# Performance work log

Measured on AMD Instinct MI355X. Metric: run time of the kernel, lower is better.

The kernel has to match this reference:

```python
import jax, jax.numpy as jnp
import numpy as np

N_NODES = 10000
N_EDGES = 160000
D_IN = 512
D_OUT = 512

def setup_inputs() -> dict:
    key = jax.random.key(0)
    k1, k2, k3, k4, k5 = jax.random.split(key, 5)
    feature = jax.random.normal(k1, (N_NODES, D_IN), dtype=jnp.float32)
    src = jax.random.randint(k2, (N_EDGES,), 0, N_NODES, dtype=jnp.int64)
    dst = jax.random.randint(k3, (N_EDGES,), 0, N_NODES, dtype=jnp.int64)
    # Linear(2*in_feats -> out_feats): stored as [2*D_IN, D_OUT] for x @ W + b
    W = jax.random.normal(k4, (2 * D_IN, D_OUT), dtype=jnp.float32) * (1.0 / np.sqrt(2 * D_IN))
    b = jax.random.normal(k5, (D_OUT,), dtype=jnp.float32) * 0.01
    return {"feature": feature, "src": src, "dst": dst, "W": W, "b": b}

def reference(feature, src, dst, W, b):
    n = feature.shape[0]
    # update_all(copy_src('h'), sum -> 'neigh'): scatter-add src features onto dst
    neigh = jax.ops.segment_sum(feature[src], dst, num_segments=n)  # [N, D_IN]
    # in_degrees(): count of incoming edges per node
    degs = jax.ops.segment_sum(jnp.ones_like(dst, dtype=feature.dtype), dst, num_segments=n)
    # clamp to 1 to avoid 0/0 for isolated nodes (sum is 0 there, so result is 0 either way)
    hk_neigh = neigh / jnp.maximum(degs, 1.0)[:, None]
    hk = jnp.concatenate([feature, hk_neigh], axis=-1) @ W + b  # [N, D_OUT]
    return jax.nn.relu(hk)
```

## Files before the change

kernel.cpp:

```cpp
#include <hip/hip_runtime.h>
#include <hip/hip_bf16.h>


#define N_NODES 10000
#define N_EDGES 160000
#define D_IN    512
#define D_OUT   512
#define K_DIM   1024

typedef float  f32x4  __attribute__((ext_vector_type(4)));
typedef __bf16 bf16x8 __attribute__((ext_vector_type(8)));
typedef unsigned short us8 __attribute__((ext_vector_type(8)));
typedef unsigned short us4 __attribute__((ext_vector_type(4)));

__device__ __forceinline__ unsigned short f2b(float f) {
    unsigned int u = __float_as_uint(f);
    unsigned int r = u + 0x7FFFu + ((u >> 16) & 1u);
    return (unsigned short)(r >> 16);
}
__device__ __forceinline__ float b2f(unsigned short h) {
    return __uint_as_float(((unsigned int)h) << 16);
}
__device__ __forceinline__ void gl_lds16(const void* g, void* l) {
    auto gp = (const __attribute__((address_space(1))) unsigned int*)(uintptr_t)g;
    auto lp = (__attribute__((address_space(3))) unsigned int*)(uintptr_t)l;
    __builtin_amdgcn_global_load_lds(gp, lp, 16, 0, 0);
}

__global__ __launch_bounds__(256) void wtrans_kernel(const float* __restrict__ W,
                                                     unsigned short* __restrict__ WbT,
                                                     int* __restrict__ cnt) {
    const int kt = blockIdx.x;
    const int nt = blockIdx.y;
    const int t  = threadIdx.x;

    const int bid = nt * 32 + kt;
    const int zi  = bid * 20 + t;
    if (t < 20 && zi < N_NODES) cnt[zi] = 0;

    __shared__ float tile[32][33];
    const int c  = t & 31;
    const int r0 = t >> 5;
#pragma unroll
    for (int p = 0; p < 4; ++p) {
        int r = r0 + p * 8;
        tile[r][c] = W[(size_t)(kt * 32 + r) * D_OUT + nt * 32 + c];
    }
    __syncthreads();
#pragma unroll
    for (int p = 0; p < 4; ++p) {
        int r = r0 + p * 8;
        WbT[(size_t)(nt * 32 + r) * K_DIM + kt * 32 + c] = f2b(tile[c][r]);
    }
}

__global__ __launch_bounds__(256) void convert_hist_kernel(const float* __restrict__ feat,
                                                           const int* __restrict__ dst,
                                                           unsigned short* __restrict__ Xb,
                                                           int* __restrict__ cnt) {
    const int gid = blockIdx.x * 256 + threadIdx.x;
    const int row = gid >> 6;
    const int l   = gid & 63;
    const float4* s = (const float4*)(feat + (size_t)row * D_IN + l * 8);
    float4 v0 = s[0], v1 = s[1];
    us8 o;
    o[0] = f2b(v0.x); o[1] = f2b(v0.y); o[2] = f2b(v0.z); o[3] = f2b(v0.w);
    o[4] = f2b(v1.x); o[5] = f2b(v1.y); o[6] = f2b(v1.z); o[7] = f2b(v1.w);
    *(us8*)(Xb + (size_t)row * K_DIM + l * 8) = o;
    if (gid < N_EDGES) atomicAdd(&cnt[dst[gid]], 1);
}

__global__ __launch_bounds__(256) void scan_kernel(const int* __restrict__ cnt,
                                                   int* __restrict__ rowstart,
                                                   int* __restrict__ cursor) {
    __shared__ int sums[256];
    const int t = threadIdx.x;
    const int base = t * 40;
    const int4* c4 = (const int4*)(cnt + base);
    int s = 0;
    if (base < N_NODES) {
#pragma unroll
        for (int i = 0; i < 10; ++i) {
            int4 v = c4[i];
            s += v.x + v.y + v.z + v.w;
        }
    }
    sums[t] = s;
    __syncthreads();
    for (int off = 1; off < 256; off <<= 1) {
        int v = (t >= off) ? sums[t - off] : 0;
        __syncthreads();
        sums[t] += v;
        __syncthreads();
    }
    int run = (t == 0) ? 0 : sums[t - 1];
    if (base < N_NODES) {
        int4* r4 = (int4*)(rowstart + base);
        int4* u4 = (int4*)(cursor + base);
#pragma unroll
        for (int i = 0; i < 10; ++i) {
            int4 v = c4[i];
            int4 o;
            o.x = run;  o.y = run + v.x;  o.z = run + v.x + v.y;
            o.w = run + v.x + v.y + v.z;
            run += v.x + v.y + v.z + v.w;
            r4[i] = o;
            u4[i] = o;
        }
    }
    if (t == 255) rowstart[N_NODES] = sums[255];
}

__global__ __launch_bounds__(256) void bucket_kernel(const int* __restrict__ src,
                                                     const int* __restrict__ dst,
                                                     int* __restrict__ cursor,
                                                     int* __restrict__ eidx) {
    int e = blockIdx.x * 256 + threadIdx.x;
    int d = dst[e];
    int slot = atomicAdd(&cursor[d], 1);
    eidx[slot] = src[e];
}

__global__ __launch_bounds__(256) void gather_kernel(unsigned short* Xb,
                                                     const int* __restrict__ eidx,
                                                     const int* __restrict__ rowstart) {
    const int wv   = threadIdx.x >> 6;
    const int l    = threadIdx.x & 63;
    const int half = (blockIdx.x >= 2500) ? 1 : 0;
    const int b    = blockIdx.x - half * 2500;
    const int node = b * 4 + wv;
    const int col  = half * 256 + l * 4;
    const int beg  = rowstart[node];
    const int end  = rowstart[node + 1];
    float a0 = 0.f, a1 = 0.f, a2 = 0.f, a3 = 0.f;
    int j = beg;
    for (; j + 8 <= end; j += 8) {
        us4 v0 = *(const us4*)(Xb + (size_t)eidx[j]     * K_DIM + col);
        us4 v1 = *(const us4*)(Xb + (size_t)eidx[j + 1] * K_DIM + col);
        us4 v2 = *(const us4*)(Xb + (size_t)eidx[j + 2] * K_DIM + col);
        us4 v3 = *(const us4*)(Xb + (size_t)eidx[j + 3] * K_DIM + col);
        us4 v4 = *(const us4*)(Xb + (size_t)eidx[j + 4] * K_DIM + col);
        us4 v5 = *(const us4*)(Xb + (size_t)eidx[j + 5] * K_DIM + col);
        us4 v6 = *(const us4*)(Xb + (size_t)eidx[j + 6] * K_DIM + col);
        us4 v7 = *(const us4*)(Xb + (size_t)eidx[j + 7] * K_DIM + col);
        a0 += ((b2f(v0[0]) + b2f(v1[0])) + (b2f(v2[0]) + b2f(v3[0])))
            + ((b2f(v4[0]) + b2f(v5[0])) + (b2f(v6[0]) + b2f(v7[0])));
        a1 += ((b2f(v0[1]) + b2f(v1[1])) + (b2f(v2[1]) + b2f(v3[1])))
            + ((b2f(v4[1]) + b2f(v5[1])) + (b2f(v6[1]) + b2f(v7[1])));
        a2 += ((b2f(v0[2]) + b2f(v1[2])) + (b2f(v2[2]) + b2f(v3[2])))
            + ((b2f(v4[2]) + b2f(v5[2])) + (b2f(v6[2]) + b2f(v7[2])));
        a3 += ((b2f(v0[3]) + b2f(v1[3])) + (b2f(v2[3]) + b2f(v3[3])))
            + ((b2f(v4[3]) + b2f(v5[3])) + (b2f(v6[3]) + b2f(v7[3])));
    }
    for (; j < end; ++j) {
        us4 v0 = *(const us4*)(Xb + (size_t)eidx[j] * K_DIM + col);
        a0 += b2f(v0[0]); a1 += b2f(v0[1]); a2 += b2f(v0[2]); a3 += b2f(v0[3]);
    }
    float sc = 1.0f / fmaxf((float)(end - beg), 1.0f);
    us4 o;
    o[0] = f2b(a0 * sc); o[1] = f2b(a1 * sc); o[2] = f2b(a2 * sc); o[3] = f2b(a3 * sc);
    *(us4*)(Xb + (size_t)node * K_DIM + D_IN + col) = o;
}

__global__ __launch_bounds__(256, 3) void gemm_kernel(const unsigned short* __restrict__ Xb,
                                                      const unsigned short* __restrict__ WbT,
                                                      const float* __restrict__ bias,
                                                      float* __restrict__ out) {
    __shared__ __align__(16) unsigned short As[2][8192];
    __shared__ __align__(16) unsigned short Bs[2][4096];

    const int p    = blockIdx.x;
    const int xcd  = p & 7;
    const int rank = p >> 3;
    const int g    = xcd + 8 * (rank >> 3);
    const int c    = rank & 7;
    if (g >= 79) return;
    const int brow = g * 128;
    const int bcol = c * 64;

    const int tid = threadIdx.x;
    const int l   = tid & 63;
    const int w   = tid >> 6;
    const int wr  = w >> 1, wc = w & 1;

    const int sub  = l >> 3;
    const int scol = ((l & 7) * 16) ^ (sub * 16);
    const char* pa[4];
    const char* pb[2];
#pragma unroll
    for (int q = 0; q < 4; ++q) {
        int ra = brow + q * 32 + w * 8 + sub;
        ra = ra < N_NODES ? ra : N_NODES - 1;
        pa[q] = (const char*)Xb + (size_t)ra * 2048 + scol;
    }
#pragma unroll
    for (int q = 0; q < 2; ++q)
        pb[q] = (const char*)WbT + (size_t)(bcol + q * 32 + w * 8 + sub) * 2048 + scol;

#define STAGE(buf, koff) do {                                          \
        gl_lds16(pa[0] + (koff), &As[buf][(0 * 32 + w * 8) * 64]);     \
        gl_lds16(pa[1] + (koff), &As[buf][(1 * 32 + w * 8) * 64]);     \
        gl_lds16(pa[2] + (koff), &As[buf][(2 * 32 + w * 8) * 64]);     \
        gl_lds16(pa[3] + (koff), &As[buf][(3 * 32 + w * 8) * 64]);     \
        gl_lds16(pb[0] + (koff), &Bs[buf][(0 * 32 + w * 8) * 64]);     \
        gl_lds16(pb[1] + (koff), &Bs[buf][(1 * 32 + w * 8) * 64]);     \
    } while (0)

    const int fr = l & 15;
    const int gq = l >> 4;
    const int sw = (fr & 7) * 16;
    const int h0 = ((gq * 16)      ^ sw) >> 1;
    const int h1 = ((64 + gq * 16) ^ sw) >> 1;

    f32x4 acc[4][2] = {};

    STAGE(0, 0);
    __syncthreads();
    int cur = 0;
#pragma unroll 2
    for (int t = 0; t < 16; ++t) {
        if (t < 15) STAGE(cur ^ 1, (t + 1) * 128);
        bf16x8 a[4][2], b[2][2];
#pragma unroll
        for (int m = 0; m < 4; ++m) {
            int r = (wr * 64 + m * 16 + fr) * 64;
            a[m][0] = *(const bf16x8*)&As[cur][r + h0];
            a[m][1] = *(const bf16x8*)&As[cur][r + h1];
        }
#pragma unroll
        for (int n = 0; n < 2; ++n) {
            int r = (wc * 32 + n * 16 + fr) * 64;
            b[n][0] = *(const bf16x8*)&Bs[cur][r + h0];
            b[n][1] = *(const bf16x8*)&Bs[cur][r + h1];
        }
#pragma unroll
        for (int kh = 0; kh < 2; ++kh)
#pragma unroll
            for (int m = 0; m < 4; ++m)
#pragma unroll
                for (int n = 0; n < 2; ++n)
                    acc[m][n] = __builtin_amdgcn_mfma_f32_16x16x32_bf16(a[m][kh], b[n][kh], acc[m][n], 0, 0, 0);
        __syncthreads();
        cur ^= 1;
    }
#undef STAGE

#pragma unroll
    for (int n = 0; n < 2; ++n) {
        int col = bcol + wc * 32 + n * 16 + fr;
        float bv = bias[col];
#pragma unroll
        for (int m = 0; m < 4; ++m) {
            int row0 = brow + wr * 64 + m * 16 + gq * 4;
#pragma unroll
            for (int j = 0; j < 4; ++j) {
                int row = row0 + j;
                if (row < N_NODES)
                    out[(size_t)row * D_OUT + col] = fmaxf(acc[m][n][j] + bv, 0.0f);
            }
        }
    }
}

extern "C" void kernel_launch(void* const* d_in, const int* in_sizes, int n_in,
                              void* d_out, int out_size, void* d_ws, size_t ws_size,
                              hipStream_t stream) {
    const float* feat = (const float*)d_in[0];
    const int*   src  = (const int*)d_in[1];
    const int*   dst  = (const int*)d_in[2];
    const float* W    = (const float*)d_in[3];
    const float* bias = (const float*)d_in[4];
    float*       out  = (float*)d_out;

    char* ws = (char*)d_ws;
    unsigned short* Xb  = (unsigned short*)(ws);
    int*   cnt          = (int*)(ws + 20480000);
    int*   rowstart     = (int*)(ws + 20520000);
    int*   cursor       = (int*)(ws + 20560016);
    int*   eidx         = (int*)(ws + 20600032);
    unsigned short* WbT = (unsigned short*)(ws + 21240032);

    wtrans_kernel<<<dim3(32, 16), 256, 0, stream>>>(W, WbT, cnt);
    convert_hist_kernel<<<2500, 256, 0, stream>>>(feat, dst, Xb, cnt);
    scan_kernel<<<1, 256, 0, stream>>>(cnt, rowstart, cursor);
    bucket_kernel<<<N_EDGES / 256, 256, 0, stream>>>(src, dst, cursor, eidx);
    gather_kernel<<<5000, 256, 0, stream>>>(Xb, eidx, rowstart);
    gemm_kernel<<<640, 256, 0, stream>>>(Xb, WbT, bias, out);
}
```

Baseline: 86.07 us.

## Fuse prefix scan into bucket kernel with per-block redundant LDS scan

Merges the single-block scan kernel and the edge bucketing kernel into one launch. Every block recomputes the full exclusive prefix sum of the degree counts in shared memory and uses it to place edges, with a separate zero-initialised cursor array. This removes one kernel launch and the serial single-block dependency, at the cost of redundant scan work per block and about 40KB of LDS per block, which limits occupancy.

```diff
diff --git a/kernel.cpp b/kernel.cpp
--- a/kernel.cpp
+++ b/kernel.cpp
@@ -35,8 +35,8 @@
     const int t  = threadIdx.x;
 
     const int bid = nt * 32 + kt;
-    const int zi  = bid * 20 + t;
-    if (t < 20 && zi < N_NODES) cnt[zi] = 0;
+    const int zi  = bid * 40 + t;
+    if (t < 40 && zi < 2 * N_NODES) cnt[zi] = 0;
 
     __shared__ float tile[32][33];
     const int c  = t & 31;
@@ -70,54 +70,54 @@
     if (gid < N_EDGES) atomicAdd(&cnt[dst[gid]], 1);
 }
 
-__global__ __launch_bounds__(256) void scan_kernel(const int* __restrict__ cnt,
-                                                   int* __restrict__ rowstart,
-                                                   int* __restrict__ cursor) {
+__global__ __launch_bounds__(256) void scanbucket_kernel(const int* __restrict__ src,
+                                                         const int* __restrict__ dst,
+                                                         const int* __restrict__ cnt,
+                                                         int* __restrict__ rowstart,
+                                                         int* __restrict__ cur,
+                                                         int* __restrict__ eidx) {
+    __shared__ int rs[N_NODES];
     __shared__ int sums[256];
     const int t = threadIdx.x;
     const int base = t * 40;
-    const int4* c4 = (const int4*)(cnt + base);
+
+    int4 v[10];
     int s = 0;
     if (base < N_NODES) {
-#pragma unroll
-        for (int i = 0; i < 10; ++i) {
-            int4 v = c4[i];
-            s += v.x + v.y + v.z + v.w;
-        }
+        const int4* c4 = (const int4*)(cnt + base);
+#pragma unroll
+        for (int i = 0; i < 10; ++i) v[i] = c4[i];
+#pragma unroll
+        for (int i = 0; i < 10; ++i) s += v[i].x + v[i].y + v[i].z + v[i].w;
     }
     sums[t] = s;
     __syncthreads();
     for (int off = 1; off < 256; off <<= 1) {
-        int v = (t >= off) ? sums[t - off] : 0;
+        int x = (t >= off) ? sums[t - off] : 0;
         __syncthreads();
-        sums[t] += v;
+        sums[t] += x;
         __syncthreads();
     }
     int run = (t == 0) ? 0 : sums[t - 1];
     if (base < N_NODES) {
-        int4* r4 = (int4*)(rowstart + base);
-        int4* u4 = (int4*)(cursor + base);
 #pragma unroll
         for (int i = 0; i < 10; ++i) {
-            int4 v = c4[i];
-            int4 o;
-            o.x = run;  o.y = run + v.x;  o.z = run + v.x + v.y;
-            o.w = run + v.x + v.y + v.z;
-            run += v.x + v.y + v.z + v.w;
-            r4[i] = o;
-            u4[i] = o;
-        }
-    }
-    if (t == 255) rowstart[N_NODES] = sums[255];
-}
-
-__global__ __launch_bounds__(256) void bucket_kernel(const int* __restrict__ src,
-                                                     const int* __restrict__ dst,
-                                                     int* __restrict__ cursor,
-                                                     int* __restrict__ eidx) {
-    int e = blockIdx.x * 256 + threadIdx.x;
-    int d = dst[e];
-    int slot = atomicAdd(&cursor[d], 1);
+            rs[base + i * 4 + 0] = run; run += v[i].x;
+            rs[base + i * 4 + 1] = run; run += v[i].y;
+            rs[base + i * 4 + 2] = run; run += v[i].z;
+            rs[base + i * 4 + 3] = run; run += v[i].w;
+        }
+    }
+    __syncthreads();
+
+    if (blockIdx.x == 0) {
+        for (int i = t; i < N_NODES; i += 256) rowstart[i] = rs[i];
+        if (t == 0) rowstart[N_NODES] = N_EDGES;
+    }
+
+    const int e = blockIdx.x * 256 + t;
+    const int d = dst[e];
+    const int slot = rs[d] + atomicAdd(&cur[d], 1);
     eidx[slot] = src[e];
 }
 
@@ -275,15 +275,15 @@
     char* ws = (char*)d_ws;
     unsigned short* Xb  = (unsigned short*)(ws);
     int*   cnt          = (int*)(ws + 20480000);
-    int*   rowstart     = (int*)(ws + 20520000);
-    int*   cursor       = (int*)(ws + 20560016);
+    int*   cur          = (int*)(ws + 20520000);
+    int*   rowstart     = (int*)(ws + 20560016);
     int*   eidx         = (int*)(ws + 20600032);
     unsigned short* WbT = (unsigned short*)(ws + 21240032);
 
     wtrans_kernel<<<dim3(32, 16), 256, 0, stream>>>(W, WbT, cnt);
     convert_hist_kernel<<<2500, 256, 0, stream>>>(feat, dst, Xb, cnt);
-    scan_kernel<<<1, 256, 0, stream>>>(cnt, rowstart, cursor);
-    bucket_kernel<<<N_EDGES / 256, 256, 0, stream>>>(src, dst, cursor, eidx);
+    scanbucket_kernel<<<N_EDGES / 256, 256, 0, stream>>>(src, dst, cnt,
+                                                         rowstart, cur, eidx);
     gather_kernel<<<5000, 256, 0, stream>>>(Xb, eidx, rowstart);
     gemm_kernel<<<640, 256, 0, stream>>>(Xb, WbT, bias, out);
 }
```

Measured after the change: 81.45 us. -5.4%, faster.
